# Kernel tuning notes

Measured on AMD Instinct MI355X. Metric: run time of the kernel, lower is better.

The kernel has to match this reference:

```python
import jax, jax.numpy as jnp
import numpy as np

B, T, C = 16, 4096, 1024
MAX_POS, PAD_IDX = 8192, 1


def setup_inputs() -> dict:
    key = jax.random.key(0)
    ks = jax.random.split(key, 6)
    x = jax.random.normal(ks[0], (B, T, C), dtype=jnp.float32)
    lengths = jax.random.randint(ks[1], (B,), 1, T, dtype=jnp.int32)
    padding_mask = jnp.arange(T, dtype=jnp.int32)[None, :] >= lengths[:, None]
    bos_emb = jax.random.normal(ks[2], (C,), dtype=jnp.float32) * 0.02
    eos_emb = jax.random.normal(ks[3], (C,), dtype=jnp.float32) * 0.02
    pos_table = jax.random.normal(ks[4], (MAX_POS + PAD_IDX + 1, C), dtype=jnp.float32) * 0.02
    pos_table = pos_table.at[PAD_IDX].set(0.0)  # padding_idx row is zero in nn.Embedding
    ln_weight = jnp.ones((C,), dtype=jnp.float32)
    ln_bias = jnp.zeros((C,), dtype=jnp.float32)
    return {"x": x, "padding_mask": padding_mask, "lengths": lengths,
            "bos_emb": bos_emb, "eos_emb": eos_emb, "pos_table": pos_table,
            "ln_weight": ln_weight, "ln_bias": ln_bias}


def reference(x, padding_mask, lengths, bos_emb, eos_emb, pos_table, ln_weight, ln_bias):
    b, t, c = x.shape
    # prepend BOS, append a zero slot  -> (B, T+2, C)
    x = jnp.concatenate([
        jnp.broadcast_to(bos_emb, (b, 1, c)).astype(x.dtype),
        x,
        jnp.zeros((b, 1, c), dtype=x.dtype),
    ], axis=1)
    # vectorized per-row EOS scatter: x[i, lengths[i]+1, :] = eos_emb
    x = x.at[jnp.arange(b), lengths + 1].set(eos_emb.astype(x.dtype))
    new_lengths = lengths + 2
    pad_mask = jnp.arange(t + 2, dtype=jnp.int32)[None, :] >= new_lengths[:, None]  # (B, T+2)
    # fairseq make_positions on padding_mask.long() with padding_idx=1:
    # mask = input.ne(padding_idx) -> non-pad; positions = cumsum(mask)*mask + padding_idx
    nonpad = (~pad_mask).astype(jnp.int32)
    positions = jnp.cumsum(nonpad, axis=1) * nonpad + PAD_IDX  # pad slots -> index 1 (zero row)
    pos = pos_table[positions]  # (B, T+2, C)
    y = x + pos
    # LayerNorm over C, eps=1e-5
    mu = jnp.mean(y, axis=-1, keepdims=True)
    var = jnp.mean(jnp.square(y - mu), axis=-1, keepdims=True)
    y = (y - mu) * jax.lax.rsqrt(var + 1e-5) * ln_weight + ln_bias
    return y, pad_mask, new_lengths
```

## Files before the change

### kernel.cpp

```cpp
#include <hip/hip_runtime.h>
#include <hip/hip_bf16.h>

#define B_ 16
#define T_ 4096
#define C_ 1024
#define TP2 (T_ + 2)

__global__ __launch_bounds__(256) void embed_ln_kernel(
    const float* __restrict__ x,
    const int*   __restrict__ lengths,
    const float* __restrict__ bos,
    const float* __restrict__ eos,
    const float* __restrict__ pos_table,
    const float* __restrict__ ln_w,
    const float* __restrict__ ln_b,
    float* __restrict__ out_y,
    float* __restrict__ out_mask,
    float* __restrict__ out_len)
{
    const int row = blockIdx.x;
    const int b   = row / TP2;
    const int t   = row - b * TP2;
    const int L   = lengths[b];
    const int tid = threadIdx.x;

    float4 v;
    if (t == 0) {
        v = reinterpret_cast<const float4*>(bos)[tid];
    } else if (t == L + 1) {
        v = reinterpret_cast<const float4*>(eos)[tid];
    } else if (t <= T_) {
        const float* src = x + (size_t)(b * T_ + (t - 1)) * C_;
        v = reinterpret_cast<const float4*>(src)[tid];
    } else {
        v = make_float4(0.f, 0.f, 0.f, 0.f);
    }

    if (t <= L + 1) {
        const float* pr = pos_table + (size_t)(t + 2) * C_;
        float4 p = reinterpret_cast<const float4*>(pr)[tid];
        v.x += p.x; v.y += p.y; v.z += p.z; v.w += p.w;
    }

    float s  = v.x + v.y + v.z + v.w;
    float ss = v.x * v.x + v.y * v.y + v.z * v.z + v.w * v.w;
    #pragma unroll
    for (int off = 32; off > 0; off >>= 1) {
        s  += __shfl_down(s,  off);
        ss += __shfl_down(ss, off);
    }
    __shared__ float sh_s[4], sh_ss[4];
    const int wave = tid >> 6;
    if ((tid & 63) == 0) { sh_s[wave] = s; sh_ss[wave] = ss; }
    __syncthreads();
    const float tot  = sh_s[0] + sh_s[1] + sh_s[2] + sh_s[3];
    const float tot2 = sh_ss[0] + sh_ss[1] + sh_ss[2] + sh_ss[3];
    const float inv_c = 1.0f / (float)C_;
    const float mu   = tot * inv_c;
    const float var  = tot2 * inv_c - mu * mu;
    const float rstd = rsqrtf(var + 1e-5f);

    const float4 w  = reinterpret_cast<const float4*>(ln_w)[tid];
    const float4 bb = reinterpret_cast<const float4*>(ln_b)[tid];
    float4 o;
    o.x = (v.x - mu) * rstd * w.x + bb.x;
    o.y = (v.y - mu) * rstd * w.y + bb.y;
    o.z = (v.z - mu) * rstd * w.z + bb.z;
    o.w = (v.w - mu) * rstd * w.w + bb.w;
    reinterpret_cast<float4*>(out_y + (size_t)row * C_)[tid] = o;

    if (tid == 0) {
        out_mask[row] = (t >= L + 2) ? 1.0f : 0.0f;
        if (t == 0) out_len[b] = (float)(L + 2);
    }
}

extern "C" void kernel_launch(void* const* d_in, const int* in_sizes, int n_in,
                              void* d_out, int out_size, void* d_ws, size_t ws_size,
                              hipStream_t stream) {
    const float* x         = (const float*)d_in[0];
    const int*   lengths   = (const int*)d_in[2];
    const float* bos       = (const float*)d_in[3];
    const float* eos       = (const float*)d_in[4];
    const float* pos_table = (const float*)d_in[5];
    const float* ln_w      = (const float*)d_in[6];
    const float* ln_b      = (const float*)d_in[7];

    float* out_y    = (float*)d_out;
    float* out_mask = out_y + (size_t)B_ * TP2 * C_;
    float* out_len  = out_mask + (size_t)B_ * TP2;

    const int grid = B_ * TP2;
    embed_ln_kernel<<<grid, 256, 0, stream>>>(
        x, lengths, bos, eos, pos_table, ln_w, ln_b,
        out_y, out_mask, out_len);
}
```

Before: 110.5 us.

## Map one wavefront per row and use nontemporal loads/stores

Each 64-lane wavefront now normalizes a full 1024-element row, with four rows per 256-thread block. The reductions become pure xor shuffles, so the shared-memory exchange and __syncthreads are gone. The x reads and output writes use nontemporal hints to keep streaming traffic from polluting cache. The grid becomes NROWS/4 (16*4098 divides by 4 exactly), and each thread holds 16 floats instead of 4.

Measured after the change: 102.8 us. 1.07x faster.

```diff
diff --git a/kernel.cpp b/kernel.cpp
--- a/kernel.cpp
+++ b/kernel.cpp
@@ -5,6 +5,9 @@
 #define T_ 4096
 #define C_ 1024
 #define TP2 (T_ + 2)
+#define NROWS (B_ * TP2)
+
+typedef float float4v __attribute__((ext_vector_type(4)));
 
 __global__ __launch_bounds__(256) void embed_ln_kernel(
     const float* __restrict__ x,
@@ -18,58 +21,65 @@
     float* __restrict__ out_mask,
     float* __restrict__ out_len)
 {
-    const int row = blockIdx.x;
-    const int b   = row / TP2;
-    const int t   = row - b * TP2;
-    const int L   = lengths[b];
-    const int tid = threadIdx.x;
+    const int row  = blockIdx.x * 4 + (threadIdx.x >> 6);
+    const int lane = threadIdx.x & 63;
+    const int b    = row / TP2;
+    const int t    = row - b * TP2;
+    const int L    = lengths[b];
 
-    float4 v;
-    if (t == 0) {
-        v = reinterpret_cast<const float4*>(bos)[tid];
-    } else if (t == L + 1) {
-        v = reinterpret_cast<const float4*>(eos)[tid];
-    } else if (t <= T_) {
-        const float* src = x + (size_t)(b * T_ + (t - 1)) * C_;
-        v = reinterpret_cast<const float4*>(src)[tid];
+    float4v v[4];
+    const float4v* srcv = nullptr;
+    if (t == 0)          srcv = reinterpret_cast<const float4v*>(bos);
+    else if (t == L + 1) srcv = reinterpret_cast<const float4v*>(eos);
+    else if (t <= T_)    srcv = reinterpret_cast<const float4v*>(
+                                    x + (size_t)(b * T_ + (t - 1)) * C_);
+    if (srcv) {
+        #pragma unroll
+        for (int i = 0; i < 4; ++i)
+            v[i] = __builtin_nontemporal_load(&srcv[i * 64 + lane]);
     } else {
-        v = make_float4(0.f, 0.f, 0.f, 0.f);
+        #pragma unroll
+        for (int i = 0; i < 4; ++i)
+            v[i] = (float4v)(0.f);
     }
 
     if (t <= L + 1) {
-        const float* pr = pos_table + (size_t)(t + 2) * C_;
-        float4 p = reinterpret_cast<const float4*>(pr)[tid];
-        v.x += p.x; v.y += p.y; v.z += p.z; v.w += p.w;
+        const float4v* pr = reinterpret_cast<const float4v*>(
+                                pos_table + (size_t)(t + 2) * C_);
+        #pragma unroll
+        for (int i = 0; i < 4; ++i)
+            v[i] += pr[i * 64 + lane];
     }
 
-    float s  = v.x + v.y + v.z + v.w;
-    float ss = v.x * v.x + v.y * v.y + v.z * v.z + v.w * v.w;
+    float s = 0.f, ss = 0.f;
+    #pragma unroll
+    for (int i = 0; i < 4; ++i) {
+        s  += v[i].x + v[i].y + v[i].z + v[i].w;
+        ss += v[i].x * v[i].x + v[i].y * v[i].y
+            + v[i].z * v[i].z + v[i].w * v[i].w;
+    }
     #pragma unroll
     for (int off = 32; off > 0; off >>= 1) {
-        s  += __shfl_down(s,  off);
-        ss += __shfl_down(ss, off);
+        s  += __shfl_xor(s,  off);
+        ss += __shfl_xor(ss, off);
     }
-    __shared__ float sh_s[4], sh_ss[4];
-    const int wave = tid >> 6;
-    if ((tid & 63) == 0) { sh_s[wave] = s; sh_ss[wave] = ss; }
-    __syncthreads();
-    const float tot  = sh_s[0] + sh_s[1] + sh_s[2] + sh_s[3];
-    const float tot2 = sh_ss[0] + sh_ss[1] + sh_ss[2] + sh_ss[3];
     const float inv_c = 1.0f / (float)C_;
-    const float mu   = tot * inv_c;
-    const float var  = tot2 * inv_c - mu * mu;
-    const float rstd = rsqrtf(var + 1e-5f);
+    const float mu    = s * inv_c;
+    const float var   = ss * inv_c - mu * mu;
+    const float rstd  = rsqrtf(var + 1e-5f);
 
-    const float4 w  = reinterpret_cast<const float4*>(ln_w)[tid];
-    const float4 bb = reinterpret_cast<const float4*>(ln_b)[tid];
-    float4 o;
-    o.x = (v.x - mu) * rstd * w.x + bb.x;
-    o.y = (v.y - mu) * rstd * w.y + bb.y;
-    o.z = (v.z - mu) * rstd * w.z + bb.z;
-    o.w = (v.w - mu) * rstd * w.w + bb.w;
-    reinterpret_cast<float4*>(out_y + (size_t)row * C_)[tid] = o;
+    float4v* dst = reinterpret_cast<float4v*>(out_y + (size_t)row * C_);
+    const float4v* wv = reinterpret_cast<const float4v*>(ln_w);
+    const float4v* bv = reinterpret_cast<const float4v*>(ln_b);
+    #pragma unroll
+    for (int i = 0; i < 4; ++i) {
+        const float4v w  = wv[i * 64 + lane];
+        const float4v bb = bv[i * 64 + lane];
+        float4v o = (v[i] - mu) * rstd * w + bb;
+        __builtin_nontemporal_store(o, &dst[i * 64 + lane]);
+    }
 
-    if (tid == 0) {
+    if (lane == 0) {
         out_mask[row] = (t >= L + 2) ? 1.0f : 0.0f;
         if (t == 0) out_len[b] = (float)(L + 2);
     }
@@ -90,7 +100,7 @@
     float* out_mask = out_y + (size_t)B_ * TP2 * C_;
     float* out_len  = out_mask + (size_t)B_ * TP2;
 
-    const int grid = B_ * TP2;
+    const int grid = NROWS / 4;
     embed_ln_kernel<<<grid, 256, 0, stream>>>(
         x, lengths, bos, eos, pos_table, ln_w, ln_b,
         out_y, out_mask, out_len);
```
